# Kernel optimization log

Measured on AMD Instinct MI355X. Metric: run time of the kernel, lower is better.

Reference implementation:

```python
import jax, jax.numpy as jnp
import numpy as np

B, S = 128, 512
VOCAB, E, H, T = 100000, 100, 128, 10  # tagset_size=10 -> CRF over T-1=9 tags
HD = H // 2  # per-direction LSTM hidden


def setup_inputs():
    key = jax.random.key(0)
    ks = jax.random.split(key, 14)
    s = 0.08
    inputs = jax.random.randint(ks[0], (B, S), 1, VOCAB)
    tags = jax.random.randint(ks[1], (B, S), 1, T)  # valid after tags-1 shift
    mask = jnp.ones((B, S), dtype=bool)
    emb = (jax.random.normal(ks[2], (VOCAB, E)) * s).at[0].set(0.0)  # padding_idx=0 row zeroed
    Wih_f = jax.random.normal(ks[3], (4 * HD, E)) * s
    Whh_f = jax.random.normal(ks[4], (4 * HD, HD)) * s
    b_f = jax.random.normal(ks[5], (4 * HD,)) * s
    Wih_b = jax.random.normal(ks[6], (4 * HD, E)) * s
    Whh_b = jax.random.normal(ks[7], (4 * HD, HD)) * s
    b_b = jax.random.normal(ks[8], (4 * HD,)) * s
    W_out = jax.random.normal(ks[9], (T, H)) * s
    b_out = jax.random.normal(ks[10], (T,)) * s
    start = jax.random.normal(ks[11], (T - 1,)) * s
    end = jax.random.normal(ks[12], (T - 1,)) * s
    trans = jax.random.normal(ks[13], (T - 1, T - 1)) * s
    return dict(inputs=inputs, tags=tags, mask=mask, emb=emb,
                Wih_f=Wih_f, Whh_f=Whh_f, b_f=b_f,
                Wih_b=Wih_b, Whh_b=Whh_b, b_b=b_b,
                W_out=W_out, b_out=b_out, start=start, end=end, trans=trans)


def _lstm_dir(x, Wih, Whh, b, reverse):
    # x: [S, B, E] time-major; PyTorch gate order i,f,g,o; b = b_ih + b_hh
    h0 = jnp.zeros((x.shape[1], Whh.shape[1]), x.dtype)

    def step(carry, xt):
        h, c = carry
        gates = xt @ Wih.T + h @ Whh.T + b
        i, f, g, o = jnp.split(gates, 4, axis=-1)
        c = jax.nn.sigmoid(f) * c + jax.nn.sigmoid(i) * jnp.tanh(g)
        h = jax.nn.sigmoid(o) * jnp.tanh(c)
        return (h, c), h

    _, hs = jax.lax.scan(step, (h0, h0), x, reverse=reverse)
    return hs  # [S, B, HD]


def _crf_nll(em, tags, mask, start, end, trans):
    # Linear-chain CRF (torchcrf-style). em: [S,B,K], tags/mask: [S,B]
    pick = lambda e, t: jnp.take_along_axis(e, t[:, None], axis=-1)[:, 0]
    # numerator: score of the gold path
    score0 = start[tags[0]] + pick(em[0], tags[0])

    def num_step(sc, inp):
        em_t, t, tp, m = inp
        return sc + jnp.where(m, trans[tp, t] + pick(em_t, t), 0.0), None

    score, _ = jax.lax.scan(num_step, score0, (em[1:], tags[1:], tags[:-1], mask[1:]))
    last_idx = mask.sum(0).astype(jnp.int32) - 1
    last_tags = jnp.take_along_axis(tags, last_idx[None, :], axis=0)[0]
    score = score + end[last_tags]
    # denominator: forward algorithm (log partition)
    alpha0 = start[None, :] + em[0]  # [B,K]

    def fwd_step(alpha, inp):
        em_t, m = inp
        nxt = jax.nn.logsumexp(alpha[:, :, None] + trans[None, :, :] + em_t[:, None, :], axis=1)
        return jnp.where(m[:, None], nxt, alpha), None

    alpha, _ = jax.lax.scan(fwd_step, alpha0, (em[1:], mask[1:]))
    logZ = jax.nn.logsumexp(alpha + end[None, :], axis=1)
    return -(score - logZ).mean()  # loss = -log_likelihood.mean()


def _forward(inputs, tags, mask, emb, Wih_f, Whh_f, b_f, Wih_b, Whh_b, b_b, W_out, b_out, start, end, trans):
    x = emb[inputs].transpose(1, 0, 2)  # [S,B,E]
    h = jnp.concatenate([_lstm_dir(x, Wih_f, Whh_f, b_f, False),
                         _lstm_dir(x, Wih_b, Whh_b, b_b, True)], axis=-1)  # [S,B,H]
    # dropout is identity at eval; slice off tag 0 as in the module
    em = (h @ W_out.T + b_out)[:, :, 1:]  # [S,B,T-1]
    return _crf_nll(em, (tags - 1).T, mask.T, start, end, trans)


def reference(inputs, tags, mask, emb, Wih_f, Whh_f, b_f, Wih_b, Whh_b, b_b, W_out, b_out, start, end, trans):
    return _forward(inputs, tags, mask, emb, Wih_f, Whh_f, b_f, Wih_b, Whh_b, b_b, W_out, b_out, start, end, trans)
```

## Files before the change

### kernel.cpp

```cpp
#include <hip/hip_runtime.h>
#include <math.h>

#define SB 512
#define NB 128
#define HD 64

typedef _Float16 h2 __attribute__((ext_vector_type(2)));
union U4 { uint4 u; h2 h[4]; _Float16 f[8]; };
union U2 { uint2 u; _Float16 f[4]; };
union UH { unsigned u; _Float16 f[2]; };

__device__ __forceinline__ float frcp(float x) { return __builtin_amdgcn_rcpf(x); }
__device__ __forceinline__ float fsig(float x) { return frcp(1.0f + __expf(-x)); }
__device__ __forceinline__ float ftanh(float x) {
    float t = __expf(-2.0f * fabsf(x));
    float r = (1.0f - t) * frcp(1.0f + t);
    return copysignf(r, x);
}
__device__ __forceinline__ float fdot2(h2 a, h2 b, float c) {
    return __builtin_amdgcn_fdot2(a, b, c, false);
}

__global__ void prep_kernel(const float* __restrict__ Wih_f, const float* __restrict__ Wih_bb,
                            const float* __restrict__ Whh_f, const float* __restrict__ Whh_bb,
                            const float* __restrict__ b_f, const float* __restrict__ b_bb,
                            const float* __restrict__ trans,
                            unsigned* __restrict__ W2h, unsigned* __restrict__ whh16,
                            float* __restrict__ bias2, float* __restrict__ Eexp)
{
    int idx = blockIdx.x * 256 + threadIdx.x;
    if (idx < 26624) {
        int col = idx / 52, d = idx - col * 52;
        int dir = col >> 8, r = col & 255, j = r >> 2, g = r & 3;
        const float* src = (dir ? Wih_bb : Wih_f) + (g * 64 + j) * 100;
        UH u; u.u = 0;
        if (d < 50) { u.f[0] = (_Float16)src[2 * d]; u.f[1] = (_Float16)src[2 * d + 1]; }
        W2h[idx] = u.u;
    } else if (idx < 43008) {
        int d = idx - 26624;
        int kp = d & 31, u = (d >> 5) & 63, g = (d >> 11) & 3, dir = d >> 13;
        const float* src = (dir ? Whh_bb : Whh_f) + (g * 64 + u) * 64 + 2 * kp;
        UH uu; uu.f[0] = (_Float16)src[0]; uu.f[1] = (_Float16)src[1];
        int k4 = kp >> 2, q = kp & 3;
        whh16[(((dir * 4 + g) * 8 + k4) * 64 + u) * 4 + q] = uu.u;
    } else if (idx < 43520) {
        int col = idx - 43008;
        int dir = col >> 8, r = col & 255, j = r >> 2, g = r & 3;
        bias2[col] = (dir ? b_bb : b_f)[g * 64 + j];
    } else if (idx < 43601) {
        int i = idx - 43520;
        Eexp[i] = __expf(trans[i]);
    }
}

__global__ __launch_bounds__(256, 1) void gemm_kernel(
    const int* __restrict__ inputs, const float* __restrict__ emb,
    const unsigned* __restrict__ W2h, const float* __restrict__ bias2,
    _Float16* __restrict__ xgh)
{
    __shared__ __align__(16) unsigned sE[128 * 52];
    __shared__ __align__(16) unsigned sW[128 * 52];
    __shared__ int stok[128];
    const int tt = blockIdx.x;
    const int tid = threadIdx.x;

    if (tid < 128) stok[tid] = inputs[tid * SB + tt];
    __syncthreads();
    for (int idx = tid; idx < 6656; idx += 256) {
        int row = idx / 52, d = idx - row * 52;
        int token = stok[row];
        UH u; u.u = 0;
        if (d < 50) {
            const float* ep = emb + (size_t)token * 100 + 2 * d;
            u.f[0] = (_Float16)ep[0]; u.f[1] = (_Float16)ep[1];
        }
        sE[idx] = u.u;
    }

    const int tx = tid & 15, ty = tid >> 4;

    for (int cb4 = 0; cb4 < 4; ++cb4) {
        const int cb = cb4 * 128;
        __syncthreads();
        for (int idx = tid; idx < 1664; idx += 256)
            ((uint4*)sW)[idx] = ((const uint4*)W2h)[cb * 13 + idx];
        __syncthreads();

        float acc[8][8];
        #pragma unroll
        for (int r = 0; r < 8; ++r)
            #pragma unroll
            for (int i = 0; i < 8; ++i) acc[r][i] = 0.f;

        for (int kk = 0; kk < 13; ++kk) {
            U4 e[8], wv[8];
            #pragma unroll
            for (int r = 0; r < 8; ++r) e[r].u = ((const uint4*)sE)[(ty + 16 * r) * 13 + kk];
            #pragma unroll
            for (int i = 0; i < 8; ++i) wv[i].u = ((const uint4*)sW)[(tx + 16 * i) * 13 + kk];
            #pragma unroll
            for (int r = 0; r < 8; ++r)
                #pragma unroll
                for (int i = 0; i < 8; ++i) {
                    float a = acc[r][i];
                    #pragma unroll
                    for (int q = 0; q < 4; ++q) a = fdot2(e[r].h[q], wv[i].h[q], a);
                    acc[r][i] = a;
                }
        }

        #pragma unroll
        for (int i = 0; i < 8; ++i) {
            int col = cb + tx + 16 * i;
            float bc = bias2[col];
            #pragma unroll
            for (int r = 0; r < 8; ++r) {
                int row = tt * NB + ty + 16 * r;
                xgh[(size_t)row * 512 + col] = (_Float16)(acc[r][i] + bc);
            }
        }
    }
}

__global__ __attribute__((amdgpu_flat_work_group_size(64, 64), amdgpu_waves_per_eu(1, 1)))
void lstm_kernel(
    const _Float16* __restrict__ xgh, const unsigned* __restrict__ whh16,
    _Float16* __restrict__ h16)
{
    const int blk = blockIdx.x;
    const int b = blk & (NB - 1);
    const int dir = blk >> 7;
    const int j = threadIdx.x;

    __shared__ __align__(16) _Float16 hbuf[64];

    U4 w0r[8], w1r[8], w2r[8], w3r[8];
    {
        const uint4* src = (const uint4*)(whh16 + dir * 8192);
        #pragma unroll
        for (int k4 = 0; k4 < 8; ++k4) w0r[k4].u = src[(0 * 8 + k4) * 64 + j];
        #pragma unroll
        for (int k4 = 0; k4 < 8; ++k4) w1r[k4].u = src[(1 * 8 + k4) * 64 + j];
        #pragma unroll
        for (int k4 = 0; k4 < 8; ++k4) w2r[k4].u = src[(2 * 8 + k4) * 64 + j];
        #pragma unroll
        for (int k4 = 0; k4 < 8; ++k4) w3r[k4].u = src[(3 * 8 + k4) * 64 + j];
    }
#define PIN4(W) asm volatile("" : "+v"((W).u.x), "+v"((W).u.y), "+v"((W).u.z), "+v"((W).u.w))
    #pragma unroll
    for (int k4 = 0; k4 < 8; ++k4) { PIN4(w0r[k4]); PIN4(w1r[k4]); PIN4(w2r[k4]); PIN4(w3r[k4]); }
#undef PIN4

    hbuf[j] = (_Float16)0.f;
    float c = 0.f;

    const int t0 = dir ? (SB - 1) : 0;
    const ptrdiff_t xstride = (dir ? -1 : 1) * (ptrdiff_t)(NB * 512);
    const _Float16* xp = xgh + ((size_t)(t0 * NB + b)) * 512 + dir * 256 + j * 4;
    _Float16* hp = h16 + ((size_t)(b * 2 + dir) * SB + t0) * 64 + j;
    const ptrdiff_t hstride = (dir ? -1 : 1) * (ptrdiff_t)64;

    U2 p0, p1, p2;
    p0.u = *(const uint2*)xp;
    p1.u = *(const uint2*)(xp + xstride);
    p2.u = *(const uint2*)(xp + 2 * xstride);
    const _Float16* xq = xp + 3 * xstride;

    for (int s = 0; s < SB; ++s) {
        float a0 = (float)p0.f[0], a1 = (float)p0.f[1];
        float a2 = (float)p0.f[2], a3 = (float)p0.f[3];
        p0 = p1; p1 = p2;
        p2.u = *(const uint2*)xq;
        xq += xstride;

        U4 hv[8];
        #pragma unroll
        for (int k4 = 0; k4 < 8; ++k4) hv[k4].u = *(const uint4*)&hbuf[k4 * 8];

        float g0[4] = {a0, 0.f, 0.f, 0.f};
        float g1[4] = {a1, 0.f, 0.f, 0.f};
        float g2[4] = {a2, 0.f, 0.f, 0.f};
        float g3[4] = {a3, 0.f, 0.f, 0.f};
        #pragma unroll
        for (int k4 = 0; k4 < 8; ++k4) {
            const int p = k4 & 3;
            #pragma unroll
            for (int q = 0; q < 4; ++q) {
                g0[p] = fdot2(hv[k4].h[q], w0r[k4].h[q], g0[p]);
                g1[p] = fdot2(hv[k4].h[q], w1r[k4].h[q], g1[p]);
                g2[p] = fdot2(hv[k4].h[q], w2r[k4].h[q], g2[p]);
                g3[p] = fdot2(hv[k4].h[q], w3r[k4].h[q], g3[p]);
            }
        }
        a0 = (g0[0] + g0[1]) + (g0[2] + g0[3]);
        a1 = (g1[0] + g1[1]) + (g1[2] + g1[3]);
        a2 = (g2[0] + g2[1]) + (g2[2] + g2[3]);
        a3 = (g3[0] + g3[1]) + (g3[2] + g3[3]);

        float ig = fsig(a0), fg = fsig(a1), gg = ftanh(a2), og = fsig(a3);
        c = fg * c + ig * gg;
        float h = og * ftanh(c);
        hbuf[j] = (_Float16)h;
        *hp = (_Float16)h;
        hp += hstride;
    }
}

__global__ __launch_bounds__(256, 1) void proj_kernel(
    const _Float16* __restrict__ h16, const float* __restrict__ W_out,
    const float* __restrict__ b_out, float* __restrict__ em3)
{
    __shared__ __align__(16) unsigned tile[128 * 64];
    __shared__ __align__(16) unsigned sWo[9 * 64];
    __shared__ float sb[9];
    const int b = blockIdx.x, tid = threadIdx.x;

    for (int i2 = tid; i2 < 576; i2 += 256) {
        int k = i2 >> 6, jp = i2 & 63;
        const float* src = W_out + (k + 1) * 128 + 2 * jp;
        UH u; u.f[0] = (_Float16)src[0]; u.f[1] = (_Float16)src[1];
        sWo[i2] = u.u;
    }
    if (tid < 9) sb[tid] = b_out[1 + tid];

    float* dst0 = em3 + (size_t)b * (SB * 12);

    for (int tt = 0; tt < 4; ++tt) {
        const int t0 = tt * 128;
        __syncthreads();
        #pragma unroll
        for (int dir = 0; dir < 2; ++dir) {
            const unsigned* src = (const unsigned*)(h16 + ((size_t)(b * 2 + dir) * SB + t0) * 64);
            for (int i = tid; i < 4096; i += 256) {
                int t = i >> 5, jp = i & 31;
                tile[t * 64 + dir * 32 + jp] = src[i];
            }
        }
        __syncthreads();

        for (int o = tid; o < 1152; o += 256) {
            int tl = o / 9, k = o - 9 * tl;
            const U4* hr = (const U4*)&tile[tl * 64];
            const U4* wr = (const U4*)&sWo[k * 64];
            float pa = 0.f, pb = 0.f;
            #pragma unroll
            for (int q = 0; q < 16; q += 2) {
                U4 hv = hr[q], wv = wr[q];
                U4 hv2 = hr[q + 1], wv2 = wr[q + 1];
                #pragma unroll
                for (int z = 0; z < 4; ++z) {
                    pa = fdot2(hv.h[z], wv.h[z], pa);
                    pb = fdot2(hv2.h[z], wv2.h[z], pb);
                }
            }
            dst0[(t0 + tl) * 12 + k] = pa + pb + sb[k];
        }
    }
}

__global__ __launch_bounds__(64, 1) void crf_gold(
    const float* __restrict__ em3, const int* __restrict__ tags,
    const float* __restrict__ startv, const float* __restrict__ endv,
    const float* __restrict__ trans, float* __restrict__ gold)
{
    const int b = blockIdx.x, l = threadIdx.x;
    const int* tb = tags + (size_t)b * SB;
    const float* eb = em3 + (size_t)b * (SB * 12);
    float sc = 0.f;
    for (int t = l; t < SB; t += 64) {
        int tg = tb[t] - 1;
        if (t > 0) {
            int tp = tb[t - 1] - 1;
            sc += trans[tp * 9 + tg] + eb[t * 12 + tg];
        }
    }
    if (l == 0) {
        int tg0 = tb[0] - 1, tgl = tb[SB - 1] - 1;
        sc += startv[tg0] + eb[tg0] + endv[tgl];
    }
    #pragma unroll
    for (int off = 32; off > 0; off >>= 1) sc += __shfl_down(sc, off);
    if (l == 0) gold[b] = sc;
}

__global__ __launch_bounds__(256, 1) void crf_scan(
    const float* __restrict__ em3, const float* __restrict__ Eexp,
    float* __restrict__ Pws)
{
    const int lane = blockIdx.x * 256 + threadIdx.x;
    const int c = lane & 31, b = lane >> 5;

    float E[81];
    #pragma unroll
    for (int i = 0; i < 81; ++i) E[i] = Eexp[i];

    float P[81];
    #pragma unroll
    for (int i = 0; i < 81; ++i) P[i] = 0.f;
    #pragma unroll
    for (int i = 0; i < 9; ++i) P[i * 9 + i] = 1.f;
    float M = 0.f;

    const int t0 = 1 + 16 * c;
    const int nst = (t0 + 16 <= SB) ? 16 : (SB - t0);
    const float* ep = em3 + (size_t)b * (SB * 12) + t0 * 12;

    for (int s = 0; s < nst; ++s, ep += 12) {
        float4 e0 = *(const float4*)ep;
        float4 e1 = *(const float4*)(ep + 4);
        float e8 = ep[8];
        float ex[9] = { __expf(e0.x), __expf(e0.y), __expf(e0.z), __expf(e0.w),
                        __expf(e1.x), __expf(e1.y), __expf(e1.z), __expf(e1.w),
                        __expf(e8) };
        #pragma unroll
        for (int i = 0; i < 9; ++i) {
            float tmp[9];
            #pragma unroll
            for (int jj = 0; jj < 9; ++jj) tmp[jj] = P[i * 9] * E[jj];
            #pragma unroll
            for (int k = 1; k < 9; ++k)
                #pragma unroll
                for (int jj = 0; jj < 9; ++jj) tmp[jj] += P[i * 9 + k] * E[k * 9 + jj];
            #pragma unroll
            for (int jj = 0; jj < 9; ++jj) P[i * 9 + jj] = tmp[jj] * ex[jj];
        }
        if ((s & 3) == 3) {
            float mx = P[0];
            #pragma unroll
            for (int i = 1; i < 81; ++i) mx = fmaxf(mx, P[i]);
            M += __logf(mx);
            float r = frcp(mx);
            #pragma unroll
            for (int i = 0; i < 81; ++i) P[i] *= r;
        }
    }

    float* dst = Pws + (size_t)lane * 84;
    #pragma unroll
    for (int i = 0; i < 81; ++i) dst[i] = P[i];
    dst[81] = M;
}

__global__ __launch_bounds__(128, 1) void crf_combine(
    const float* __restrict__ em3, const float* __restrict__ Pws,
    const float* __restrict__ gold, const float* __restrict__ startv,
    const float* __restrict__ endv, float* __restrict__ out)
{
    const int b = threadIdx.x;
    float A[9], M = 0.f;
    {
        const float* eb = em3 + (size_t)b * (SB * 12);
        float4 e0 = *(const float4*)eb;
        float4 e1 = *(const float4*)(eb + 4);
        float e[9] = { e0.x, e0.y, e0.z, e0.w, e1.x, e1.y, e1.z, e1.w, eb[8] };
        #pragma unroll
        for (int k = 0; k < 9; ++k) A[k] = __expf(startv[k] + e[k]);
    }

    for (int c = 0; c < 32; ++c) {
        const float4* src = (const float4*)(Pws + ((size_t)b * 32 + c) * 84);
        float buf[84];
        #pragma unroll
        for (int q = 0; q < 21; ++q) {
            float4 v = src[q];
            buf[4 * q] = v.x; buf[4 * q + 1] = v.y; buf[4 * q + 2] = v.z; buf[4 * q + 3] = v.w;
        }
        float tmp[9];
        #pragma unroll
        for (int jj = 0; jj < 9; ++jj) tmp[jj] = A[0] * buf[jj];
        #pragma unroll
        for (int i = 1; i < 9; ++i)
            #pragma unroll
            for (int jj = 0; jj < 9; ++jj) tmp[jj] += A[i] * buf[i * 9 + jj];
        float mx = tmp[0];
        #pragma unroll
        for (int jj = 1; jj < 9; ++jj) mx = fmaxf(mx, tmp[jj]);
        M += __logf(mx) + buf[81];
        float r = frcp(mx);
        #pragma unroll
        for (int jj = 0; jj < 9; ++jj) A[jj] = tmp[jj] * r;
    }

    float Z = 0.f;
    #pragma unroll
    for (int k = 0; k < 9; ++k) Z += A[k] * __expf(endv[k]);
    float part = M + __logf(Z) - gold[b];

    #pragma unroll
    for (int off = 32; off > 0; off >>= 1) part += __shfl_down(part, off);
    __shared__ float sm[2];
    if ((b & 63) == 0) sm[b >> 6] = part;
    __syncthreads();
    if (b == 0) out[0] = (sm[0] + sm[1]) * (1.0f / NB);
}

extern "C" void kernel_launch(void* const* d_in, const int* in_sizes, int n_in,
                              void* d_out, int out_size, void* d_ws, size_t ws_size,
                              hipStream_t stream)
{
    const int*   inputs = (const int*)d_in[0];
    const int*   tags   = (const int*)d_in[1];
    const float* emb    = (const float*)d_in[3];
    const float* Wih_f  = (const float*)d_in[4];
    const float* Whh_f  = (const float*)d_in[5];
    const float* b_f    = (const float*)d_in[6];
    const float* Wih_b  = (const float*)d_in[7];
    const float* Whh_b  = (const float*)d_in[8];
    const float* b_b    = (const float*)d_in[9];
    const float* W_out  = (const float*)d_in[10];
    const float* b_out  = (const float*)d_in[11];
    const float* startv = (const float*)d_in[12];
    const float* endv   = (const float*)d_in[13];
    const float* transv = (const float*)d_in[14];

    char* w = (char*)d_ws;
    float* em3     = (float*)w;     w += (size_t)NB * SB * 12 * 4;
    _Float16* xgh  = (_Float16*)w;  w += (size_t)SB * NB * 512 * 2;
    _Float16* h16  = (_Float16*)w;  w += (size_t)NB * 2 * SB * 64 * 2;
    float* Pws     = (float*)w;     w += (size_t)NB * 32 * 84 * 4;
    float* gold    = (float*)w;     w += NB * 4;
    unsigned* W2h  = (unsigned*)w;  w += 26624 * 4;
    unsigned* whh16= (unsigned*)w;  w += 16384 * 4;
    float* bias2   = (float*)w;     w += 512 * 4;
    float* Eexp    = (float*)w;     w += 81 * 4;

    prep_kernel<<<171, 256, 0, stream>>>(Wih_f, Wih_b, Whh_f, Whh_b, b_f, b_b, transv,
                                         W2h, whh16, bias2, Eexp);
    gemm_kernel<<<SB, 256, 0, stream>>>(inputs, emb, W2h, bias2, xgh);
    lstm_kernel<<<256, 64, 0, stream>>>(xgh, whh16, h16);
    proj_kernel<<<NB, 256, 0, stream>>>(h16, W_out, b_out, em3);
    crf_gold<<<NB, 64, 0, stream>>>(em3, tags, startv, endv, transv, gold);
    crf_scan<<<16, 256, 0, stream>>>(em3, Eexp, Pws);
    crf_combine<<<1, 128, 0, stream>>>(em3, Pws, gold, startv, endv, (float*)d_out);
}
```

Measured before the change: 547.6 us.

## Split LSTM recurrent matvec across two waves with LDS partial-sum exchange

The recurrent LSTM kernel now uses two wavefronts per (batch, direction) block. Each wave computes half of the 64-wide hidden-dot-product for all four gates, and the halves are combined through double-buffered shared memory with a barrier every step. This halves the serial FMA chain and the per-thread weight registers, aiming to shorten the latency-bound time-step loop. In exchange it adds a workgroup barrier and an LDS round trip to each of the 512 steps, and both waves redundantly compute the gate nonlinearities.

```diff
diff --git a/kernel.cpp b/kernel.cpp
--- a/kernel.cpp
+++ b/kernel.cpp
@@ -122,7 +122,7 @@
     }
 }
 
-__global__ __attribute__((amdgpu_flat_work_group_size(64, 64), amdgpu_waves_per_eu(1, 1)))
+__global__ __attribute__((amdgpu_flat_work_group_size(128, 128), amdgpu_waves_per_eu(1, 1)))
 void lstm_kernel(
     const _Float16* __restrict__ xgh, const unsigned* __restrict__ whh16,
     _Float16* __restrict__ h16)
@@ -130,28 +130,30 @@
     const int blk = blockIdx.x;
     const int b = blk & (NB - 1);
     const int dir = blk >> 7;
-    const int j = threadIdx.x;
-
-    __shared__ __align__(16) _Float16 hbuf[64];
-
-    U4 w0r[8], w1r[8], w2r[8], w3r[8];
+    const int tid = threadIdx.x;
+    const int w = tid >> 6;
+    const int j = tid & 63;
+
+    __shared__ __align__(16) float pb[2][2][64][4];
+    __shared__ __align__(16) _Float16 hb[2][64];
+
+    U4 wr[4][4];
     {
-        const uint4* src = (const uint4*)(whh16 + dir * 8192);
-        #pragma unroll
-        for (int k4 = 0; k4 < 8; ++k4) w0r[k4].u = src[(0 * 8 + k4) * 64 + j];
-        #pragma unroll
-        for (int k4 = 0; k4 < 8; ++k4) w1r[k4].u = src[(1 * 8 + k4) * 64 + j];
-        #pragma unroll
-        for (int k4 = 0; k4 < 8; ++k4) w2r[k4].u = src[(2 * 8 + k4) * 64 + j];
-        #pragma unroll
-        for (int k4 = 0; k4 < 8; ++k4) w3r[k4].u = src[(3 * 8 + k4) * 64 + j];
+        const uint4* src4 = (const uint4*)(whh16 + dir * 8192);
+        #pragma unroll
+        for (int g = 0; g < 4; ++g)
+            #pragma unroll
+            for (int i = 0; i < 4; ++i)
+                wr[g][i].u = src4[(g * 8 + 4 * w + i) * 64 + j];
     }
 #define PIN4(W) asm volatile("" : "+v"((W).u.x), "+v"((W).u.y), "+v"((W).u.z), "+v"((W).u.w))
     #pragma unroll
-    for (int k4 = 0; k4 < 8; ++k4) { PIN4(w0r[k4]); PIN4(w1r[k4]); PIN4(w2r[k4]); PIN4(w3r[k4]); }
+    for (int g = 0; g < 4; ++g)
+        #pragma unroll
+        for (int i = 0; i < 4; ++i) PIN4(wr[g][i]);
 #undef PIN4
 
-    hbuf[j] = (_Float16)0.f;
+    hb[w][j] = (_Float16)0.f;
     float c = 0.f;
 
     const int t0 = dir ? (SB - 1) : 0;
@@ -161,48 +163,63 @@
     const ptrdiff_t hstride = (dir ? -1 : 1) * (ptrdiff_t)64;
 
     U2 p0, p1, p2;
-    p0.u = *(const uint2*)xp;
-    p1.u = *(const uint2*)(xp + xstride);
-    p2.u = *(const uint2*)(xp + 2 * xstride);
     const _Float16* xq = xp + 3 * xstride;
+    if (w == 0) {
+        p0.u = *(const uint2*)xp;
+        p1.u = *(const uint2*)(xp + xstride);
+        p2.u = *(const uint2*)(xp + 2 * xstride);
+    }
 
     for (int s = 0; s < SB; ++s) {
-        float a0 = (float)p0.f[0], a1 = (float)p0.f[1];
-        float a2 = (float)p0.f[2], a3 = (float)p0.f[3];
-        p0 = p1; p1 = p2;
-        p2.u = *(const uint2*)xq;
-        xq += xstride;
-
-        U4 hv[8];
-        #pragma unroll
-        for (int k4 = 0; k4 < 8; ++k4) hv[k4].u = *(const uint4*)&hbuf[k4 * 8];
-
-        float g0[4] = {a0, 0.f, 0.f, 0.f};
-        float g1[4] = {a1, 0.f, 0.f, 0.f};
-        float g2[4] = {a2, 0.f, 0.f, 0.f};
-        float g3[4] = {a3, 0.f, 0.f, 0.f};
-        #pragma unroll
-        for (int k4 = 0; k4 < 8; ++k4) {
-            const int p = k4 & 3;
+        float a0, a1, a2, a3;
+        if (w == 0) {
+            a0 = (float)p0.f[0]; a1 = (float)p0.f[1];
+            a2 = (float)p0.f[2]; a3 = (float)p0.f[3];
+            p0 = p1; p1 = p2;
+            p2.u = *(const uint2*)xq;
+            xq += xstride;
+        } else {
+            a0 = a1 = a2 = a3 = 0.f;
+        }
+
+        U4 hv[4];
+        #pragma unroll
+        for (int i = 0; i < 4; ++i) hv[i].u = *(const uint4*)&hb[w][32 * w + 8 * i];
+
+        float s0[2] = {a0, 0.f}, s1[2] = {a1, 0.f}, s2[2] = {a2, 0.f}, s3[2] = {a3, 0.f};
+        #pragma unroll
+        for (int i = 0; i < 4; ++i) {
             #pragma unroll
             for (int q = 0; q < 4; ++q) {
-                g0[p] = fdot2(hv[k4].h[q], w0r[k4].h[q], g0[p]);
-                g1[p] = fdot2(hv[k4].h[q], w1r[k4].h[q], g1[p]);
-                g2[p] = fdot2(hv[k4].h[q], w2r[k4].h[q], g2[p]);
-                g3[p] = fdot2(hv[k4].h[q], w3r[k4].h[q], g3[p]);
+                const int p = q & 1;
+                s0[p] = fdot2(hv[i].h[q], wr[0][i].h[q], s0[p]);
+                s1[p] = fdot2(hv[i].h[q], wr[1][i].h[q], s1[p]);
+                s2[p] = fdot2(hv[i].h[q], wr[2][i].h[q], s2[p]);
+                s3[p] = fdot2(hv[i].h[q], wr[3][i].h[q], s3[p]);
             }
         }
-        a0 = (g0[0] + g0[1]) + (g0[2] + g0[3]);
-        a1 = (g1[0] + g1[1]) + (g1[2] + g1[3]);
-        a2 = (g2[0] + g2[1]) + (g2[2] + g2[3]);
-        a3 = (g3[0] + g3[1]) + (g3[2] + g3[3]);
-
-        float ig = fsig(a0), fg = fsig(a1), gg = ftanh(a2), og = fsig(a3);
+
+        const int par = s & 1;
+        *(float4*)&pb[par][w][j][0] = make_float4(s0[0] + s0[1], s1[0] + s1[1],
+                                                  s2[0] + s2[1], s3[0] + s3[1]);
+        asm volatile("s_waitcnt lgkmcnt(0)" ::: "memory");
+        __builtin_amdgcn_s_barrier();
+        asm volatile("" ::: "memory");
+        float4 o = *(const float4*)&pb[par][1 - w][j][0];
+
+        float A0 = s0[0] + s0[1] + o.x;
+        float A1 = s1[0] + s1[1] + o.y;
+        float A2 = s2[0] + s2[1] + o.z;
+        float A3 = s3[0] + s3[1] + o.w;
+
+        float ig = fsig(A0), fg = fsig(A1), gg = ftanh(A2), og = fsig(A3);
         c = fg * c + ig * gg;
         float h = og * ftanh(c);
-        hbuf[j] = (_Float16)h;
-        *hp = (_Float16)h;
-        hp += hstride;
+        hb[w][j] = (_Float16)h;
+        if (w == 0) {
+            *hp = (_Float16)h;
+            hp += hstride;
+        }
     }
 }
 
@@ -427,7 +444,7 @@
     prep_kernel<<<171, 256, 0, stream>>>(Wih_f, Wih_b, Whh_f, Whh_b, b_f, b_b, transv,
                                          W2h, whh16, bias2, Eexp);
     gemm_kernel<<<SB, 256, 0, stream>>>(inputs, emb, W2h, bias2, xgh);
-    lstm_kernel<<<256, 64, 0, stream>>>(xgh, whh16, h16);
+    lstm_kernel<<<256, 128, 0, stream>>>(xgh, whh16, h16);
     proj_kernel<<<NB, 256, 0, stream>>>(h16, W_out, b_out, em3);
     crf_gold<<<NB, 64, 0, stream>>>(em3, tags, startv, endv, transv, gold);
     crf_scan<<<16, 256, 0, stream>>>(em3, Eexp, Pws);
```

After: 562.7 us. 2.7% more time.
